# Kernel optimization log

Hardware: AMD Instinct MI355X
Metric: run time of the kernel (lower is better)

The kernel has to match this reference:

```python
import jax, jax.numpy as jnp
import numpy as np


def setup_inputs() -> dict:
    key = jax.random.key(0)
    k1, k2, k3 = jax.random.split(key, 3)
    RAW_NODES = 40962          # ico-6 sphere
    NUM_NODES = RAW_NODES * 4 - 6   # 163842, ico-7 sphere
    FEAT = 256
    x = jax.random.normal(k1, (RAW_NODES, FEAT), dtype=jnp.float32)
    max_index = jax.random.randint(k2, (RAW_NODES, FEAT), 0, 7, dtype=jnp.int64)
    neigh_orders = jax.random.randint(k3, (RAW_NODES * 7,), 0, NUM_NODES, dtype=jnp.int64)
    return {"x": x, "max_index": max_index, "neigh_orders": neigh_orders, "num_nodes": NUM_NODES}


def reference(x, max_index, neigh_orders, num_nodes):
    raw_nodes, feat_num = x.shape
    # column_ref[i, f] = i*7 + max_index[i, f]  (vectorized form of the python loop)
    column_ref = (jnp.arange(raw_nodes, dtype=max_index.dtype)[:, None] * 7 + max_index).reshape(-1)
    column_index = neigh_orders[column_ref]  # gather from neighborhood lookup table
    # row_index exactly as in the original: floor(linspace(0, feat_num, raw_nodes*feat_num)), last clamped
    row_index = np.floor(np.linspace(0.0, float(feat_num), num=raw_nodes * feat_num)).astype(np.int64)
    row_index[-1] = row_index[-1] - 1
    row_index = jnp.asarray(row_index)
    y = jnp.zeros((num_nodes, feat_num), dtype=x.dtype)
    # scatter: y[column_index, row_index] = x.view(-1)
    y = y.at[column_index, row_index].set(x.reshape(-1))
    return y
```

## Files before the change

### kernel.cpp

```cpp
#include <hip/hip_runtime.h>
#include <stdint.h>


#define FEAT 256
#define LOG2FEAT 8
#define BLOCK 256
#define NROWS 256
#define SPLIT 8
#define HASH 512
typedef float f32x4 __attribute__((ext_vector_type(4)));

extern "C" __global__ __launch_bounds__(BLOCK)
void zero_counts_kernel(int* __restrict__ count, int n)
{
    for (int idx = blockIdx.x * BLOCK + threadIdx.x; idx < n;
         idx += gridDim.x * BLOCK)
        count[idx] = 0;
}

extern "C" __global__ __launch_bounds__(BLOCK)
void row_build_kernel(const int*   __restrict__ mi,
                      const int*   __restrict__ neigh,
                      const float* __restrict__ x,
                      int2*        __restrict__ table,
                      int*         __restrict__ count,
                      int total,
                      int cap)
{
    __shared__ int hkey[HASH];
    __shared__ int hval[HASH];

    const int tid = threadIdx.x;
    for (int s = tid; s < HASH; s += BLOCK) { hkey[s] = -1; hval[s] = 0; }
    __syncthreads();

    const int r   = blockIdx.x / SPLIT;
    const int sub = blockIdx.x % SPLIT;
    const unsigned tm1 = (unsigned)(total - 1);
    const unsigned klo = ((unsigned)r * tm1 + 255u) >> 8;
    const unsigned khi = (r == 255) ? (unsigned)(total - 1)
                       : (((unsigned)(r + 1) * tm1 + 255u) >> 8) - 1u;
    const int i0 = (int)(klo >> 8);
    const int i1 = (int)(khi >> 8);
    const int len   = i1 - i0 + 1;
    const int chunk = (len + SPLIT - 1) / SPLIT;
    const int ia = i0 + sub * chunk;
    int ib = ia + chunk - 1; if (ib > i1) ib = i1;

    const int lane = tid & 63;
    const int wv   = tid >> 6;

    int p0 = 0, p1 = 0, p2 = 0, p3 = 0;
    {
        const int ifirst = ia + wv;
        if (ifirst <= ib) {
            const int* mrow = mi + (ifirst << LOG2FEAT);
            p0 = mrow[lane];       p1 = mrow[64 + lane];
            p2 = mrow[128 + lane]; p3 = mrow[192 + lane];
        }
    }

    for (int i = ia + wv; i <= ib; i += 4) {
        const int m0 = p0, m1 = p1, m2 = p2, m3 = p3;
        const int inx = i + 4;
        if (inx <= ib) {
            const int* mrow = mi + (inx << LOG2FEAT);
            p0 = mrow[lane];       p1 = mrow[64 + lane];
            p2 = mrow[128 + lane]; p3 = mrow[192 + lane];
        }
        const int mycol = (lane < 7) ? neigh[i * 7 + lane] : 0;

        const int kbase = i << LOG2FEAT;
        int wlo = (int)klo - kbase; if (wlo < 0)   wlo = 0;
        int whi = (int)khi - kbase; if (whi > 255) whi = 255;

        unsigned long long wm[4];
        #pragma unroll
        for (int j = 0; j < 4; ++j) {
            int lo = wlo - j * 64;  if (lo < 0) lo = 0;
            int hi = whi - j * 64 + 1;
            unsigned long long mhi = (hi >= 64) ? ~0ull
                                   : (hi <= 0)  ? 0ull : ((1ull << hi) - 1ull);
            unsigned long long mlo = (lo >= 64) ? ~0ull : ((1ull << lo) - 1ull);
            wm[j] = mhi & ~mlo;
        }

        unsigned long long b[4][7];
        #pragma unroll
        for (int m = 0; m < 7; ++m) {
            b[0][m] = __ballot(m0 == m);
            b[1][m] = __ballot(m1 == m);
            b[2][m] = __ballot(m2 == m);
            b[3][m] = __ballot(m3 == m);
        }

        if (lane < 7) {
            const int m = lane;
            int bestf = -1;
            #pragma unroll
            for (int j = 3; j >= 0; --j) {
                if (bestf < 0) {
                    unsigned long long s =
                        (m == 0) ? b[j][0] : (m == 1) ? b[j][1] :
                        (m == 2) ? b[j][2] : (m == 3) ? b[j][3] :
                        (m == 4) ? b[j][4] : (m == 5) ? b[j][5] : b[j][6];
                    unsigned long long t = s & wm[j];
                    if (t) bestf = j * 64 + 63 - __clzll(t);
                }
            }
            if (bestf >= 0) {
                const int kp1 = kbase + bestf + 1;
                int slot = mycol & (HASH - 1);
                while (true) {
                    int prev = atomicCAS(&hkey[slot], -1, mycol);
                    if (prev == -1 || prev == mycol) {
                        atomicMax(&hval[slot], kp1);
                        break;
                    }
                    slot = (slot + 1) & (HASH - 1);
                }
            }
        }
    }

    __syncthreads();

    for (int s = tid; s < HASH; s += BLOCK) {
        const int key = hkey[s];
        if (key >= 0) {
            const int kp1  = hval[s];
            const int bits = __float_as_int(x[kp1 - 1]);
            const int slot = atomicAdd(&count[key], 1);
            if (slot < cap)
                table[(size_t)key * cap + slot] =
                    make_int2((int)(((unsigned)kp1 << 8) | (unsigned)r), bits);
        }
    }
}

extern "C" __global__ __launch_bounds__(BLOCK)
void compose_kernel(float*      __restrict__ out,
                    const int2* __restrict__ table,
                    const int*  __restrict__ count,
                    int nnodes, int cap)
{
    const int lane   = threadIdx.x & 63;
    const int wv     = (blockIdx.x * BLOCK + threadIdx.x) >> 6;
    const int nwaves = gridDim.x * (BLOCK / 64);

    for (int n = wv; n < nnodes; n += nwaves) {
        int c = count[n];
        if (c > cap) c = cap;
        int2 e = make_int2(0, 0);
        if (lane < c) e = table[(size_t)n * cap + lane];

        unsigned k0 = 0, k1 = 0, k2 = 0, k3 = 0;
        int f0 = 0, f1 = 0, f2 = 0, f3 = 0;
        for (int j = 0; j < c; ++j) {
            const unsigned ex = (unsigned)__shfl(e.x, j);
            const int      bj = __shfl(e.y, j);
            const int      rj = (int)(ex & 255u);
            if ((rj >> 2) == lane) {
                const int q = rj & 3;
                if      (q == 0) { if (ex > k0) { k0 = ex; f0 = bj; } }
                else if (q == 1) { if (ex > k1) { k1 = ex; f1 = bj; } }
                else if (q == 2) { if (ex > k2) { k2 = ex; f2 = bj; } }
                else             { if (ex > k3) { k3 = ex; f3 = bj; } }
            }
        }
        f32x4 f;
        f.x = __int_as_float(f0); f.y = __int_as_float(f1);
        f.z = __int_as_float(f2); f.w = __int_as_float(f3);
        f32x4* dst = (f32x4*)(out + ((size_t)n << LOG2FEAT)) + lane;
        *dst = f;
    }
}

extern "C" void kernel_launch(void* const* d_in, const int* in_sizes, int n_in,
                              void* d_out, int out_size, void* d_ws, size_t ws_size,
                              hipStream_t stream) {
    const float* x     = (const float*)d_in[0];
    const int*   mi    = (const int*)d_in[1];
    const int*   neigh = (const int*)d_in[2];
    float*       out   = (float*)d_out;

    const int total  = in_sizes[0];
    const int nnodes = out_size >> LOG2FEAT;

    int cap = 32;
    while (cap > 8 &&
           (size_t)nnodes * (size_t)cap * sizeof(int2) + (size_t)nnodes * 4
               > ws_size)
        cap >>= 1;

    int2* table = (int2*)d_ws;
    int*  count = (int*)((char*)d_ws +
                         (size_t)nnodes * (size_t)cap * sizeof(int2));

    zero_counts_kernel<<<dim3(256), dim3(BLOCK), 0, stream>>>(count, nnodes);
    row_build_kernel<<<dim3(NROWS * SPLIT), dim3(BLOCK), 0, stream>>>(
        mi, neigh, x, table, count, total, cap);
    compose_kernel<<<dim3(2048), dim3(BLOCK), 0, stream>>>(
        out, table, count, nnodes, cap);
}
```

Before: 281.3 us.

## Drop LDS hash dedup, vectorize index loads, prefetch compose entries

```diff
diff --git a/kernel.cpp b/kernel.cpp
--- a/kernel.cpp
+++ b/kernel.cpp
@@ -6,8 +6,7 @@
 #define LOG2FEAT 8
 #define BLOCK 256
 #define NROWS 256
-#define SPLIT 8
-#define HASH 512
+#define SPLIT 16
 typedef float f32x4 __attribute__((ext_vector_type(4)));
 
 extern "C" __global__ __launch_bounds__(BLOCK)
@@ -27,13 +26,7 @@
                       int total,
                       int cap)
 {
-    __shared__ int hkey[HASH];
-    __shared__ int hval[HASH];
-
     const int tid = threadIdx.x;
-    for (int s = tid; s < HASH; s += BLOCK) { hkey[s] = -1; hval[s] = 0; }
-    __syncthreads();
-
     const int r   = blockIdx.x / SPLIT;
     const int sub = blockIdx.x % SPLIT;
     const unsigned tm1 = (unsigned)(total - 1);
@@ -50,90 +43,76 @@
     const int lane = tid & 63;
     const int wv   = tid >> 6;
 
-    int p0 = 0, p1 = 0, p2 = 0, p3 = 0;
+    int4 pv = make_int4(7, 7, 7, 7);
+    int  pn = 0;
     {
         const int ifirst = ia + wv;
         if (ifirst <= ib) {
-            const int* mrow = mi + (ifirst << LOG2FEAT);
-            p0 = mrow[lane];       p1 = mrow[64 + lane];
-            p2 = mrow[128 + lane]; p3 = mrow[192 + lane];
+            pv = *(const int4*)(mi + (ifirst << LOG2FEAT) + 4 * lane);
+            pn = (lane < 7) ? neigh[ifirst * 7 + lane] : 0;
         }
     }
 
     for (int i = ia + wv; i <= ib; i += 4) {
-        const int m0 = p0, m1 = p1, m2 = p2, m3 = p3;
-        const int inx = i + 4;
+        const int4 v    = pv;
+        const int mycol = pn;
+        const int inx   = i + 4;
         if (inx <= ib) {
-            const int* mrow = mi + (inx << LOG2FEAT);
-            p0 = mrow[lane];       p1 = mrow[64 + lane];
-            p2 = mrow[128 + lane]; p3 = mrow[192 + lane];
-        }
-        const int mycol = (lane < 7) ? neigh[i * 7 + lane] : 0;
+            pv = *(const int4*)(mi + (inx << LOG2FEAT) + 4 * lane);
+            pn = (lane < 7) ? neigh[inx * 7 + lane] : 0;
+        }
 
         const int kbase = i << LOG2FEAT;
         int wlo = (int)klo - kbase; if (wlo < 0)   wlo = 0;
         int whi = (int)khi - kbase; if (whi > 255) whi = 255;
 
-        unsigned long long wm[4];
+        unsigned long long M[4];
         #pragma unroll
-        for (int j = 0; j < 4; ++j) {
-            int lo = wlo - j * 64;  if (lo < 0) lo = 0;
-            int hi = whi - j * 64 + 1;
-            unsigned long long mhi = (hi >= 64) ? ~0ull
-                                   : (hi <= 0)  ? 0ull : ((1ull << hi) - 1ull);
-            unsigned long long mlo = (lo >= 64) ? ~0ull : ((1ull << lo) - 1ull);
-            wm[j] = mhi & ~mlo;
-        }
-
-        unsigned long long b[4][7];
+        for (int q = 0; q < 4; ++q) {
+            int a = wlo - q; if (a < 0) a = 0;
+            const int lo_l = (a + 3) >> 2;
+            const int b = whi - q;
+            unsigned long long mq = 0;
+            if (b >= 0 && lo_l <= 63) {
+                const int hi_l = b >> 2;
+                mq = (hi_l >= 63) ? ~0ull : ((1ull << (hi_l + 1)) - 1ull);
+                if (lo_l > 0) mq &= ~((1ull << lo_l) - 1ull);
+            }
+            M[q] = mq;
+        }
+
+        unsigned long long B[4][7];
         #pragma unroll
         for (int m = 0; m < 7; ++m) {
-            b[0][m] = __ballot(m0 == m);
-            b[1][m] = __ballot(m1 == m);
-            b[2][m] = __ballot(m2 == m);
-            b[3][m] = __ballot(m3 == m);
+            B[0][m] = __ballot(v.x == m);
+            B[1][m] = __ballot(v.y == m);
+            B[2][m] = __ballot(v.z == m);
+            B[3][m] = __ballot(v.w == m);
         }
 
         if (lane < 7) {
             const int m = lane;
             int bestf = -1;
             #pragma unroll
-            for (int j = 3; j >= 0; --j) {
-                if (bestf < 0) {
-                    unsigned long long s =
-                        (m == 0) ? b[j][0] : (m == 1) ? b[j][1] :
-                        (m == 2) ? b[j][2] : (m == 3) ? b[j][3] :
-                        (m == 4) ? b[j][4] : (m == 5) ? b[j][5] : b[j][6];
-                    unsigned long long t = s & wm[j];
-                    if (t) bestf = j * 64 + 63 - __clzll(t);
+            for (int q = 0; q < 4; ++q) {
+                const unsigned long long s =
+                    (m == 0) ? B[q][0] : (m == 1) ? B[q][1] :
+                    (m == 2) ? B[q][2] : (m == 3) ? B[q][3] :
+                    (m == 4) ? B[q][4] : (m == 5) ? B[q][5] : B[q][6];
+                const unsigned long long t = s & M[q];
+                if (t) {
+                    const int f = 4 * (63 - __clzll(t)) + q;
+                    if (f > bestf) bestf = f;
                 }
             }
             if (bestf >= 0) {
-                const int kp1 = kbase + bestf + 1;
-                int slot = mycol & (HASH - 1);
-                while (true) {
-                    int prev = atomicCAS(&hkey[slot], -1, mycol);
-                    if (prev == -1 || prev == mycol) {
-                        atomicMax(&hval[slot], kp1);
-                        break;
-                    }
-                    slot = (slot + 1) & (HASH - 1);
-                }
-            }
-        }
-    }
-
-    __syncthreads();
-
-    for (int s = tid; s < HASH; s += BLOCK) {
-        const int key = hkey[s];
-        if (key >= 0) {
-            const int kp1  = hval[s];
-            const int bits = __float_as_int(x[kp1 - 1]);
-            const int slot = atomicAdd(&count[key], 1);
-            if (slot < cap)
-                table[(size_t)key * cap + slot] =
-                    make_int2((int)(((unsigned)kp1 << 8) | (unsigned)r), bits);
+                const int kp1  = kbase + bestf + 1;
+                const int bits = __float_as_int(x[kp1 - 1]);
+                const int slot = atomicAdd(&count[mycol], 1);
+                if (slot < cap)
+                    table[(size_t)mycol * cap + slot] = make_int2(
+                        (int)(((unsigned)kp1 << 8) | (unsigned)r), bits);
+            }
         }
     }
 }
@@ -144,15 +123,33 @@
                     const int*  __restrict__ count,
                     int nnodes, int cap)
 {
-    const int lane   = threadIdx.x & 63;
-    const int wv     = (blockIdx.x * BLOCK + threadIdx.x) >> 6;
-    const int nwaves = gridDim.x * (BLOCK / 64);
-
-    for (int n = wv; n < nnodes; n += nwaves) {
-        int c = count[n];
+    const int lane = threadIdx.x & 63;
+    const int wv   = (blockIdx.x * BLOCK + threadIdx.x) >> 6;
+    const int nw   = gridDim.x * (BLOCK / 64);
+
+    int n = wv;
+    int c = 0;
+    int2 e = make_int2(0, 0);
+    if (n < nnodes) {
+        c = count[n];
+        if (lane < 8) e = table[(size_t)n * cap + lane];
+    }
+
+    while (n < nnodes) {
+        const int n2 = n + nw;
+        int c2 = 0;
+        int2 e2 = make_int2(0, 0);
+        if (n2 < nnodes) {
+            c2 = count[n2];
+            if (lane < 8) e2 = table[(size_t)n2 * cap + lane];
+        }
+
         if (c > cap) c = cap;
-        int2 e = make_int2(0, 0);
-        if (lane < c) e = table[(size_t)n * cap + lane];
+        if (c > 8) {
+            if (lane >= 8 && lane < c)
+                e = table[(size_t)n * cap + lane];
+        }
+        if (lane >= c) { e.x = 0; e.y = 0; }
 
         unsigned k0 = 0, k1 = 0, k2 = 0, k3 = 0;
         int f0 = 0, f1 = 0, f2 = 0, f3 = 0;
@@ -173,6 +170,8 @@
         f.z = __int_as_float(f2); f.w = __int_as_float(f3);
         f32x4* dst = (f32x4*)(out + ((size_t)n << LOG2FEAT)) + lane;
         *dst = f;
+
+        n = n2; c = c2; e = e2;
     }
 }
 
```

New measurement: 271.1 us. 3.6% less time.
